# Kernel tuning notes

Measured on AMD Instinct MI355X. Metric: run time of the kernel, lower is better.

## Reference

```python
import jax, jax.numpy as jnp
import numpy as np

B, N, K, C_IN, C_OUT = 4, 8192, 16, 128, 128


def setup_inputs() -> dict:
    key = jax.random.key(0)
    k1, k2, k3 = jax.random.split(key, 3)
    x = jax.random.normal(k1, (B, N, C_IN), dtype=jnp.float32)
    edge_index = jax.random.randint(k2, (2, B, N, K), 0, N, dtype=jnp.int64)
    W = jax.random.normal(k3, (C_OUT, C_IN), dtype=jnp.float32) * (1.0 / np.sqrt(C_IN))
    b = jnp.zeros((C_OUT,), dtype=jnp.float32)
    eps = jnp.zeros((1,), dtype=jnp.float32)  # eps_init = 0.0
    return {"x": x, "edge_index": edge_index, "W": W, "b": b, "eps": eps}


def reference(x, edge_index, W, b, eps):
    # x: [B, N, C], edge_index: [2, B, N, K] -- use source index edge_index[0]
    idx = edge_index[0]                                   # [B, N, K]
    # gather neighbor features per batch: x_j[b,n,k,:] = x[b, idx[b,n,k], :]
    x_j = jax.vmap(lambda xb, ib: xb[ib])(x, idx)         # [B, N, K, C]
    agg = jnp.sum(x_j, axis=2)                            # sum over neighbors -> [B, N, C]
    h = (1.0 + eps) * x + agg                             # eps-scaled residual
    # MLP([in, out], act='relu'): single linear + relu on channel dim
    out = jax.nn.relu(jnp.einsum("bnc,oc->bno", h, W) + b)
    return out
```

## Files before the change

kernel.cpp:

```cpp
#include <hip/hip_runtime.h>
#include <stdint.h>

#define BATCH   4
#define NNODE   8192
#define KNBR    16
#define CIN     128
#define COUT    128
#define MB      32
#define THREADS 256
#define HS_STRIDE 136

typedef __attribute__((ext_vector_type(8))) short short8;
typedef __attribute__((ext_vector_type(4))) float f32x4;

__device__ __forceinline__ short bf16_rne(float f) {
    union { float f; uint32_t u; } v; v.f = f;
    return (short)((v.u + 0x7FFFu + ((v.u >> 16) & 1u)) >> 16);
}
__device__ __forceinline__ float bf16_f32(short s) {
    union { uint32_t u; float f; } v; v.u = ((uint32_t)(uint16_t)s) << 16;
    return v.f;
}

__global__ __launch_bounds__(256)
void cvt_bf16(const float* __restrict__ x, ushort* __restrict__ xb) {
    const int gid = blockIdx.x * 256 + threadIdx.x;
    const f32x4* xp = (const f32x4*)x + (size_t)gid * 2;
    f32x4 a = xp[0], c = xp[1];
    short8 s;
    s[0]=bf16_rne(a[0]); s[1]=bf16_rne(a[1]); s[2]=bf16_rne(a[2]); s[3]=bf16_rne(a[3]);
    s[4]=bf16_rne(c[0]); s[5]=bf16_rne(c[1]); s[6]=bf16_rne(c[2]); s[7]=bf16_rne(c[3]);
    ((short8*)xb)[gid] = s;
}

template<bool USEBF>
__global__ __launch_bounds__(THREADS, 2)
void gin_fused(const float*  __restrict__ x,
               const ushort* __restrict__ xb,
               const int*    __restrict__ eidx,
               const float*  __restrict__ W,
               const float*  __restrict__ bias,
               const float*  __restrict__ epsp,
               float*        __restrict__ out)
{
    __shared__ __align__(16) short h_s[MB * HS_STRIDE];

    const int tid = threadIdx.x;
    const int i   = blockIdx.x;
    const int xcd = i & 7;
    const int sub = i >> 3;
    const int b   = xcd >> 1;
    const int wbi = ((xcd & 1) << 7) | sub;
    const int n0  = wbi * MB;
    const int row0 = b * NNODE + n0;

    const float eps1 = 1.0f + epsp[0];

    {
        const int r  = tid >> 3;
        const int q  = tid & 7;
        const int n  = n0 + r;
        const int c0 = q * 16;
        const int* ip = eidx + ((size_t)b * NNODE + n) * KNBR;

        int js[KNBR];
        #pragma unroll
        for (int p = 0; p < 4; ++p) {
            int4 jv = *(const int4*)(ip + p * 4);
            js[p*4+0]=jv.x; js[p*4+1]=jv.y; js[p*4+2]=jv.z; js[p*4+3]=jv.w;
        }

        float acc[16];

        if constexpr (USEBF) {
            const ushort* xbb = xb + (size_t)b * NNODE * CIN;
            const ushort* xs  = xbb + (size_t)n * CIN + c0;
            short8 s0 = *(const short8*)xs, s1 = *(const short8*)(xs + 8);

            short8 t0[KNBR], t1[KNBR];
            #pragma unroll
            for (int k = 0; k < KNBR; ++k) {
                const ushort* xn = xbb + (size_t)js[k] * CIN + c0;
                t0[k] = *(const short8*)xn;
                t1[k] = *(const short8*)(xn + 8);
            }

            #pragma unroll
            for (int e = 0; e < 8; ++e) {
                acc[e]     = eps1 * bf16_f32(s0[e]);
                acc[8 + e] = eps1 * bf16_f32(s1[e]);
            }
            #pragma unroll
            for (int k = 0; k < KNBR; ++k) {
                #pragma unroll
                for (int e = 0; e < 8; ++e) {
                    acc[e]     += bf16_f32(t0[k][e]);
                    acc[8 + e] += bf16_f32(t1[k][e]);
                }
            }
        } else {
            const float* xbb = x + (size_t)b * NNODE * CIN;
            const float* xs  = xbb + (size_t)n * CIN + c0;
            #pragma unroll
            for (int p = 0; p < 4; ++p) {
                f32x4 v = *(const f32x4*)(xs + p * 4);
                acc[p*4+0]=eps1*v[0]; acc[p*4+1]=eps1*v[1]; acc[p*4+2]=eps1*v[2]; acc[p*4+3]=eps1*v[3];
            }
            #pragma unroll
            for (int k = 0; k < KNBR; ++k) {
                const float* xn = xbb + (size_t)js[k] * CIN + c0;
                #pragma unroll
                for (int p = 0; p < 4; ++p) {
                    f32x4 v = *(const f32x4*)(xn + p * 4);
                    acc[p*4+0]+=v[0]; acc[p*4+1]+=v[1]; acc[p*4+2]+=v[2]; acc[p*4+3]+=v[3];
                }
            }
        }

        short* hp = h_s + r * HS_STRIDE + c0;
        #pragma unroll
        for (int p = 0; p < 2; ++p) {
            short8 s;
            #pragma unroll
            for (int e = 0; e < 8; ++e) s[e] = bf16_rne(acc[p*8+e]);
            *(short8*)(hp + p * 8) = s;
        }
    }

    const int wave = tid >> 6;
    const int lane = tid & 63;
    const int l16  = lane & 15;
    const int lq   = lane >> 4;

    short8 bfrag[2][4];
    #pragma unroll
    for (int t = 0; t < 2; ++t) {
        const float* wp = W + (size_t)(wave * 32 + t * 16 + l16) * CIN;
        #pragma unroll
        for (int kb = 0; kb < 4; ++kb) {
            const float* wq = wp + kb * 32 + lq * 8;
            f32x4 f0 = *(const f32x4*)(wq);
            f32x4 f1 = *(const f32x4*)(wq + 4);
            short8 s;
            s[0]=bf16_rne(f0[0]); s[1]=bf16_rne(f0[1]); s[2]=bf16_rne(f0[2]); s[3]=bf16_rne(f0[3]);
            s[4]=bf16_rne(f1[0]); s[5]=bf16_rne(f1[1]); s[6]=bf16_rne(f1[2]); s[7]=bf16_rne(f1[3]);
            bfrag[t][kb] = s;
        }
    }
    const float bias0 = bias[wave * 32 + l16];
    const float bias1 = bias[wave * 32 + 16 + l16];

    __syncthreads();

    float* outb = out + (size_t)row0 * COUT;
    #pragma unroll
    for (int rt = 0; rt < MB / 16; ++rt) {
        const short* ap = h_s + (rt * 16 + l16) * HS_STRIDE + lq * 8;
        short8 afrag[4];
        #pragma unroll
        for (int kb = 0; kb < 4; ++kb)
            afrag[kb] = *(const short8*)(ap + kb * 32);

        #pragma unroll
        for (int t = 0; t < 2; ++t) {
            f32x4 acc = { 0.f, 0.f, 0.f, 0.f };
            #pragma unroll
            for (int kb = 0; kb < 4; ++kb)
                acc = __builtin_amdgcn_mfma_f32_16x16x32_bf16(afrag[kb], bfrag[t][kb], acc, 0, 0, 0);

            const float bv  = t ? bias1 : bias0;
            const int   col = wave * 32 + t * 16 + l16;
            #pragma unroll
            for (int ii = 0; ii < 4; ++ii) {
                const int row = rt * 16 + lq * 4 + ii;
                float v = acc[ii] + bv;
                outb[(size_t)row * COUT + col] = v > 0.f ? v : 0.f;
            }
        }
    }
}

extern "C" void kernel_launch(void* const* d_in, const int* in_sizes, int n_in,
                              void* d_out, int out_size, void* d_ws, size_t ws_size,
                              hipStream_t stream) {
    const float* x    = (const float*)d_in[0];
    const int*   eidx = (const int*)d_in[1];
    const float* W    = (const float*)d_in[2];
    const float* bias = (const float*)d_in[3];
    const float* eps  = (const float*)d_in[4];
    float*       out  = (float*)d_out;

    const size_t need = (size_t)BATCH * NNODE * CIN * sizeof(ushort);
    dim3 grid((BATCH * NNODE) / MB);

    if (ws_size >= need) {
        ushort* xb = (ushort*)d_ws;
        const int nelem = BATCH * NNODE * CIN;
        cvt_bf16<<<dim3(nelem / (256 * 8)), dim3(256), 0, stream>>>(x, xb);
        gin_fused<true><<<grid, dim3(THREADS), 0, stream>>>(x, xb, eidx, W, bias, eps, out);
    } else {
        gin_fused<false><<<grid, dim3(THREADS), 0, stream>>>(x, nullptr, eidx, W, bias, eps, out);
    }
}
```

Measured before the change: 95.73 us.

## Drop bf16 pre-conversion pass and gather fp32 neighbors in two batched halves

Removes the separate kernel that converted x to bf16 in workspace and always gathers neighbor rows directly in fp32. Neighbor loads are issued in two batches of eight rows, holding 32 vector registers of loads in flight before accumulating. This saves a full read and write pass over x and one kernel launch, but doubles the bytes fetched per gathered neighbor and raises register pressure.

```diff
diff --git a/kernel.cpp b/kernel.cpp
--- a/kernel.cpp
+++ b/kernel.cpp
@@ -17,31 +17,14 @@
     union { float f; uint32_t u; } v; v.f = f;
     return (short)((v.u + 0x7FFFu + ((v.u >> 16) & 1u)) >> 16);
 }
-__device__ __forceinline__ float bf16_f32(short s) {
-    union { uint32_t u; float f; } v; v.u = ((uint32_t)(uint16_t)s) << 16;
-    return v.f;
-}
 
-__global__ __launch_bounds__(256)
-void cvt_bf16(const float* __restrict__ x, ushort* __restrict__ xb) {
-    const int gid = blockIdx.x * 256 + threadIdx.x;
-    const f32x4* xp = (const f32x4*)x + (size_t)gid * 2;
-    f32x4 a = xp[0], c = xp[1];
-    short8 s;
-    s[0]=bf16_rne(a[0]); s[1]=bf16_rne(a[1]); s[2]=bf16_rne(a[2]); s[3]=bf16_rne(a[3]);
-    s[4]=bf16_rne(c[0]); s[5]=bf16_rne(c[1]); s[6]=bf16_rne(c[2]); s[7]=bf16_rne(c[3]);
-    ((short8*)xb)[gid] = s;
-}
-
-template<bool USEBF>
 __global__ __launch_bounds__(THREADS, 2)
-void gin_fused(const float*  __restrict__ x,
-               const ushort* __restrict__ xb,
-               const int*    __restrict__ eidx,
-               const float*  __restrict__ W,
-               const float*  __restrict__ bias,
-               const float*  __restrict__ epsp,
-               float*        __restrict__ out)
+void gin_fused_f32(const float*  __restrict__ x,
+                   const int*    __restrict__ eidx,
+                   const float*  __restrict__ W,
+                   const float*  __restrict__ bias,
+                   const float*  __restrict__ epsp,
+                   float*        __restrict__ out)
 {
     __shared__ __align__(16) short h_s[MB * HS_STRIDE];
 
@@ -70,49 +53,32 @@
             js[p*4+0]=jv.x; js[p*4+1]=jv.y; js[p*4+2]=jv.z; js[p*4+3]=jv.w;
         }
 
+        const float* xbb = x + (size_t)b * NNODE * CIN;
+        const float* xs  = xbb + (size_t)n * CIN + c0;
+
         float acc[16];
+        #pragma unroll
+        for (int p = 0; p < 4; ++p) {
+            f32x4 v = *(const f32x4*)(xs + p * 4);
+            acc[p*4+0]=eps1*v[0]; acc[p*4+1]=eps1*v[1];
+            acc[p*4+2]=eps1*v[2]; acc[p*4+3]=eps1*v[3];
+        }
 
-        if constexpr (USEBF) {
-            const ushort* xbb = xb + (size_t)b * NNODE * CIN;
-            const ushort* xs  = xbb + (size_t)n * CIN + c0;
-            short8 s0 = *(const short8*)xs, s1 = *(const short8*)(xs + 8);
-
-            short8 t0[KNBR], t1[KNBR];
+        #pragma unroll
+        for (int h = 0; h < 2; ++h) {
+            f32x4 t[8][4];
             #pragma unroll
-            for (int k = 0; k < KNBR; ++k) {
-                const ushort* xn = xbb + (size_t)js[k] * CIN + c0;
-                t0[k] = *(const short8*)xn;
-                t1[k] = *(const short8*)(xn + 8);
-            }
-
-            #pragma unroll
-            for (int e = 0; e < 8; ++e) {
-                acc[e]     = eps1 * bf16_f32(s0[e]);
-                acc[8 + e] = eps1 * bf16_f32(s1[e]);
+            for (int k = 0; k < 8; ++k) {
+                const float* xn = xbb + (size_t)js[h*8+k] * CIN + c0;
+                #pragma unroll
+                for (int p = 0; p < 4; ++p) t[k][p] = *(const f32x4*)(xn + p * 4);
             }
             #pragma unroll
-            for (int k = 0; k < KNBR; ++k) {
-                #pragma unroll
-                for (int e = 0; e < 8; ++e) {
-                    acc[e]     += bf16_f32(t0[k][e]);
-                    acc[8 + e] += bf16_f32(t1[k][e]);
-                }
-            }
-        } else {
-            const float* xbb = x + (size_t)b * NNODE * CIN;
-            const float* xs  = xbb + (size_t)n * CIN + c0;
-            #pragma unroll
-            for (int p = 0; p < 4; ++p) {
-                f32x4 v = *(const f32x4*)(xs + p * 4);
-                acc[p*4+0]=eps1*v[0]; acc[p*4+1]=eps1*v[1]; acc[p*4+2]=eps1*v[2]; acc[p*4+3]=eps1*v[3];
-            }
-            #pragma unroll
-            for (int k = 0; k < KNBR; ++k) {
-                const float* xn = xbb + (size_t)js[k] * CIN + c0;
+            for (int k = 0; k < 8; ++k) {
                 #pragma unroll
                 for (int p = 0; p < 4; ++p) {
-                    f32x4 v = *(const f32x4*)(xn + p * 4);
-                    acc[p*4+0]+=v[0]; acc[p*4+1]+=v[1]; acc[p*4+2]+=v[2]; acc[p*4+3]+=v[3];
+                    acc[p*4+0] += t[k][p][0]; acc[p*4+1] += t[k][p][1];
+                    acc[p*4+2] += t[k][p][2]; acc[p*4+3] += t[k][p][3];
                 }
             }
         }
@@ -190,15 +156,8 @@
     const float* eps  = (const float*)d_in[4];
     float*       out  = (float*)d_out;
 
-    const size_t need = (size_t)BATCH * NNODE * CIN * sizeof(ushort);
+    (void)d_ws; (void)ws_size;
+
     dim3 grid((BATCH * NNODE) / MB);
-
-    if (ws_size >= need) {
-        ushort* xb = (ushort*)d_ws;
-        const int nelem = BATCH * NNODE * CIN;
-        cvt_bf16<<<dim3(nelem / (256 * 8)), dim3(256), 0, stream>>>(x, xb);
-        gin_fused<true><<<grid, dim3(THREADS), 0, stream>>>(x, xb, eidx, W, bias, eps, out);
-    } else {
-        gin_fused<false><<<grid, dim3(THREADS), 0, stream>>>(x, nullptr, eidx, W, bias, eps, out);
-    }
+    gin_fused_f32<<<grid, dim3(THREADS), 0, stream>>>(x, eidx, W, bias, eps, out);
 }
```

New measurement: 113.6 us. 1.19x slower.

## Halve node tile to 16 rows, raise occupancy, add nontemporal loads/stores

Applied to the files above, without the earlier changes.

Shrinks the per-block node tile from 32 to 16 rows, so each thread gathers 8 channels instead of 16 and holds half as many neighbor vectors in registers. Launch bounds rise from 2 to 4 blocks per CU to allow more waves in flight to hide gather latency, and the XCD-aware block mapping is widened to match the doubled grid. The conversion kernel's input loads and the output stores are made nontemporal, and a sched_barrier keeps all gather loads issued before the accumulation. The trade-off is that every block now reloads and converts the full weight matrix for half as many rows, and there are more, smaller blocks.

```diff
diff --git a/kernel.cpp b/kernel.cpp
--- a/kernel.cpp
+++ b/kernel.cpp
@@ -6,7 +6,7 @@
 #define KNBR    16
 #define CIN     128
 #define COUT    128
-#define MB      32
+#define MB      16
 #define THREADS 256
 #define HS_STRIDE 136
 
@@ -26,7 +26,8 @@
 void cvt_bf16(const float* __restrict__ x, ushort* __restrict__ xb) {
     const int gid = blockIdx.x * 256 + threadIdx.x;
     const f32x4* xp = (const f32x4*)x + (size_t)gid * 2;
-    f32x4 a = xp[0], c = xp[1];
+    f32x4 a = __builtin_nontemporal_load(xp);
+    f32x4 c = __builtin_nontemporal_load(xp + 1);
     short8 s;
     s[0]=bf16_rne(a[0]); s[1]=bf16_rne(a[1]); s[2]=bf16_rne(a[2]); s[3]=bf16_rne(a[3]);
     s[4]=bf16_rne(c[0]); s[5]=bf16_rne(c[1]); s[6]=bf16_rne(c[2]); s[7]=bf16_rne(c[3]);
@@ -34,7 +35,7 @@
 }
 
 template<bool USEBF>
-__global__ __launch_bounds__(THREADS, 2)
+__global__ __launch_bounds__(THREADS, 4)
 void gin_fused(const float*  __restrict__ x,
                const ushort* __restrict__ xb,
                const int*    __restrict__ eidx,
@@ -50,17 +51,17 @@
     const int xcd = i & 7;
     const int sub = i >> 3;
     const int b   = xcd >> 1;
-    const int wbi = ((xcd & 1) << 7) | sub;
+    const int wbi = ((xcd & 1) << 8) | sub;
     const int n0  = wbi * MB;
     const int row0 = b * NNODE + n0;
 
     const float eps1 = 1.0f + epsp[0];
 
     {
-        const int r  = tid >> 3;
-        const int q  = tid & 7;
+        const int r  = tid >> 4;
+        const int q  = tid & 15;
         const int n  = n0 + r;
-        const int c0 = q * 16;
+        const int c0 = q * 8;
         const int* ip = eidx + ((size_t)b * NNODE + n) * KNBR;
 
         int js[KNBR];
@@ -70,61 +71,47 @@
             js[p*4+0]=jv.x; js[p*4+1]=jv.y; js[p*4+2]=jv.z; js[p*4+3]=jv.w;
         }
 
-        float acc[16];
+        float acc[8];
 
         if constexpr (USEBF) {
             const ushort* xbb = xb + (size_t)b * NNODE * CIN;
-            const ushort* xs  = xbb + (size_t)n * CIN + c0;
-            short8 s0 = *(const short8*)xs, s1 = *(const short8*)(xs + 8);
+            short8 s0 = *(const short8*)(xbb + (size_t)n * CIN + c0);
 
-            short8 t0[KNBR], t1[KNBR];
+            short8 t[KNBR];
             #pragma unroll
-            for (int k = 0; k < KNBR; ++k) {
-                const ushort* xn = xbb + (size_t)js[k] * CIN + c0;
-                t0[k] = *(const short8*)xn;
-                t1[k] = *(const short8*)(xn + 8);
-            }
+            for (int k = 0; k < KNBR; ++k)
+                t[k] = *(const short8*)(xbb + (size_t)js[k] * CIN + c0);
+            __builtin_amdgcn_sched_barrier(0);
 
             #pragma unroll
-            for (int e = 0; e < 8; ++e) {
-                acc[e]     = eps1 * bf16_f32(s0[e]);
-                acc[8 + e] = eps1 * bf16_f32(s1[e]);
-            }
+            for (int e = 0; e < 8; ++e) acc[e] = eps1 * bf16_f32(s0[e]);
             #pragma unroll
             for (int k = 0; k < KNBR; ++k) {
                 #pragma unroll
-                for (int e = 0; e < 8; ++e) {
-                    acc[e]     += bf16_f32(t0[k][e]);
-                    acc[8 + e] += bf16_f32(t1[k][e]);
-                }
+                for (int e = 0; e < 8; ++e) acc[e] += bf16_f32(t[k][e]);
             }
         } else {
             const float* xbb = x + (size_t)b * NNODE * CIN;
             const float* xs  = xbb + (size_t)n * CIN + c0;
+            f32x4 v0 = *(const f32x4*)(xs);
+            f32x4 v1 = *(const f32x4*)(xs + 4);
             #pragma unroll
-            for (int p = 0; p < 4; ++p) {
-                f32x4 v = *(const f32x4*)(xs + p * 4);
-                acc[p*4+0]=eps1*v[0]; acc[p*4+1]=eps1*v[1]; acc[p*4+2]=eps1*v[2]; acc[p*4+3]=eps1*v[3];
-            }
+            for (int e = 0; e < 4; ++e) { acc[e] = eps1*v0[e]; acc[4+e] = eps1*v1[e]; }
             #pragma unroll
             for (int k = 0; k < KNBR; ++k) {
                 const float* xn = xbb + (size_t)js[k] * CIN + c0;
+                f32x4 w0 = *(const f32x4*)(xn);
+                f32x4 w1 = *(const f32x4*)(xn + 4);
                 #pragma unroll
-                for (int p = 0; p < 4; ++p) {
-                    f32x4 v = *(const f32x4*)(xn + p * 4);
-                    acc[p*4+0]+=v[0]; acc[p*4+1]+=v[1]; acc[p*4+2]+=v[2]; acc[p*4+3]+=v[3];
-                }
+                for (int e = 0; e < 4; ++e) { acc[e] += w0[e]; acc[4+e] += w1[e]; }
             }
         }
 
         short* hp = h_s + r * HS_STRIDE + c0;
+        short8 s;
         #pragma unroll
-        for (int p = 0; p < 2; ++p) {
-            short8 s;
-            #pragma unroll
-            for (int e = 0; e < 8; ++e) s[e] = bf16_rne(acc[p*8+e]);
-            *(short8*)(hp + p * 8) = s;
-        }
+        for (int e = 0; e < 8; ++e) s[e] = bf16_rne(acc[e]);
+        *(short8*)hp = s;
     }
 
     const int wave = tid >> 6;
@@ -153,9 +140,8 @@
     __syncthreads();
 
     float* outb = out + (size_t)row0 * COUT;
-    #pragma unroll
-    for (int rt = 0; rt < MB / 16; ++rt) {
-        const short* ap = h_s + (rt * 16 + l16) * HS_STRIDE + lq * 8;
+    {
+        const short* ap = h_s + l16 * HS_STRIDE + lq * 8;
         short8 afrag[4];
         #pragma unroll
         for (int kb = 0; kb < 4; ++kb)
@@ -172,9 +158,10 @@
             const int   col = wave * 32 + t * 16 + l16;
             #pragma unroll
             for (int ii = 0; ii < 4; ++ii) {
-                const int row = rt * 16 + lq * 4 + ii;
+                const int row = lq * 4 + ii;
                 float v = acc[ii] + bv;
-                outb[(size_t)row * COUT + col] = v > 0.f ? v : 0.f;
+                v = v > 0.f ? v : 0.f;
+                __builtin_nontemporal_store(v, &outb[(size_t)row * COUT + col]);
             }
         }
     }
```

Result: slower. 101.7 us (+6.3%).

## Merge bf16 conversion and gather-GEMM into one persistent kernel with grid barrier

Applied to the files above, without the earlier changes.

Replaces the separate bf16 conversion kernel and the fused gather/MLP kernel with a single 512-block kernel. Each block converts its slice of x to bf16, waits on a global atomic barrier, then processes two 32-node tiles using the existing gather plus MFMA path. Nontemporal loads and stores are added for x, indices and output. The change removes one kernel launch and its inter-kernel gap. In exchange it relies on all 512 blocks being co-resident, since the software grid barrier deadlocks otherwise, and it halves the number of blocks that can hide gather latency.

```diff
diff --git a/kernel.cpp b/kernel.cpp
--- a/kernel.cpp
+++ b/kernel.cpp
@@ -6,12 +6,15 @@
 #define KNBR    16
 #define CIN     128
 #define COUT    128
-#define MB      32
 #define THREADS 256
+#define GRID    512
 #define HS_STRIDE 136
+
+#define XELEM   (BATCH * NNODE * CIN)
 
 typedef __attribute__((ext_vector_type(8))) short short8;
 typedef __attribute__((ext_vector_type(4))) float f32x4;
+typedef __attribute__((ext_vector_type(4))) int   i32x4;
 
 __device__ __forceinline__ short bf16_rne(float f) {
     union { float f; uint32_t u; } v; v.f = f;
@@ -22,108 +25,39 @@
     return v.f;
 }
 
-__global__ __launch_bounds__(256)
-void cvt_bf16(const float* __restrict__ x, ushort* __restrict__ xb) {
-    const int gid = blockIdx.x * 256 + threadIdx.x;
-    const f32x4* xp = (const f32x4*)x + (size_t)gid * 2;
-    f32x4 a = xp[0], c = xp[1];
-    short8 s;
-    s[0]=bf16_rne(a[0]); s[1]=bf16_rne(a[1]); s[2]=bf16_rne(a[2]); s[3]=bf16_rne(a[3]);
-    s[4]=bf16_rne(c[0]); s[5]=bf16_rne(c[1]); s[6]=bf16_rne(c[2]); s[7]=bf16_rne(c[3]);
-    ((short8*)xb)[gid] = s;
-}
-
-template<bool USEBF>
+__device__ unsigned long long g_bar;
+
 __global__ __launch_bounds__(THREADS, 2)
-void gin_fused(const float*  __restrict__ x,
-               const ushort* __restrict__ xb,
-               const int*    __restrict__ eidx,
-               const float*  __restrict__ W,
-               const float*  __restrict__ bias,
-               const float*  __restrict__ epsp,
-               float*        __restrict__ out)
+void gin_mono(const float* __restrict__ x,
+              const int*   __restrict__ eidx,
+              const float* __restrict__ W,
+              const float* __restrict__ bias,
+              const float* __restrict__ epsp,
+              ushort*      __restrict__ xb,
+              float*       __restrict__ out)
 {
-    __shared__ __align__(16) short h_s[MB * HS_STRIDE];
-
-    const int tid = threadIdx.x;
-    const int i   = blockIdx.x;
-    const int xcd = i & 7;
-    const int sub = i >> 3;
-    const int b   = xcd >> 1;
-    const int wbi = ((xcd & 1) << 7) | sub;
-    const int n0  = wbi * MB;
-    const int row0 = b * NNODE + n0;
-
-    const float eps1 = 1.0f + epsp[0];
+    __shared__ __align__(16) short h_s[32 * HS_STRIDE];
+
+    const int tid  = threadIdx.x;
+    const int i    = blockIdx.x;
+    const int xcd  = i & 7;
+    const int sub  = i >> 3;
+    const int b    = xcd >> 1;
+    const int half = xcd & 1;
+    const int chunk = half * 64 + sub;
 
     {
-        const int r  = tid >> 3;
-        const int q  = tid & 7;
-        const int n  = n0 + r;
-        const int c0 = q * 16;
-        const int* ip = eidx + ((size_t)b * NNODE + n) * KNBR;
-
-        int js[KNBR];
-        #pragma unroll
-        for (int p = 0; p < 4; ++p) {
-            int4 jv = *(const int4*)(ip + p * 4);
-            js[p*4+0]=jv.x; js[p*4+1]=jv.y; js[p*4+2]=jv.z; js[p*4+3]=jv.w;
-        }
-
-        float acc[16];
-
-        if constexpr (USEBF) {
-            const ushort* xbb = xb + (size_t)b * NNODE * CIN;
-            const ushort* xs  = xbb + (size_t)n * CIN + c0;
-            short8 s0 = *(const short8*)xs, s1 = *(const short8*)(xs + 8);
-
-            short8 t0[KNBR], t1[KNBR];
-            #pragma unroll
-            for (int k = 0; k < KNBR; ++k) {
-                const ushort* xn = xbb + (size_t)js[k] * CIN + c0;
-                t0[k] = *(const short8*)xn;
-                t1[k] = *(const short8*)(xn + 8);
-            }
-
-            #pragma unroll
-            for (int e = 0; e < 8; ++e) {
-                acc[e]     = eps1 * bf16_f32(s0[e]);
-                acc[8 + e] = eps1 * bf16_f32(s1[e]);
-            }
-            #pragma unroll
-            for (int k = 0; k < KNBR; ++k) {
-                #pragma unroll
-                for (int e = 0; e < 8; ++e) {
-                    acc[e]     += bf16_f32(t0[k][e]);
-                    acc[8 + e] += bf16_f32(t1[k][e]);
-                }
-            }
-        } else {
-            const float* xbb = x + (size_t)b * NNODE * CIN;
-            const float* xs  = xbb + (size_t)n * CIN + c0;
-            #pragma unroll
-            for (int p = 0; p < 4; ++p) {
-                f32x4 v = *(const f32x4*)(xs + p * 4);
-                acc[p*4+0]=eps1*v[0]; acc[p*4+1]=eps1*v[1]; acc[p*4+2]=eps1*v[2]; acc[p*4+3]=eps1*v[3];
-            }
-            #pragma unroll
-            for (int k = 0; k < KNBR; ++k) {
-                const float* xn = xbb + (size_t)js[k] * CIN + c0;
-                #pragma unroll
-                for (int p = 0; p < 4; ++p) {
-                    f32x4 v = *(const f32x4*)(xn + p * 4);
-                    acc[p*4+0]+=v[0]; acc[p*4+1]+=v[1]; acc[p*4+2]+=v[2]; acc[p*4+3]+=v[3];
-                }
-            }
-        }
-
-        short* hp = h_s + r * HS_STRIDE + c0;
-        #pragma unroll
-        for (int p = 0; p < 2; ++p) {
+        const size_t base = ((size_t)b * NNODE + (size_t)chunk * 64) * CIN;
+        const float*  xs = x  + base + tid * 32;
+        ushort*       xd = xb + base + tid * 32;
+        #pragma unroll
+        for (int g = 0; g < 4; ++g) {
+            f32x4 a = __builtin_nontemporal_load((const f32x4*)(xs + g * 8));
+            f32x4 c = __builtin_nontemporal_load((const f32x4*)(xs + g * 8 + 4));
             short8 s;
-            #pragma unroll
-            for (int e = 0; e < 8; ++e) s[e] = bf16_rne(acc[p*8+e]);
-            *(short8*)(hp + p * 8) = s;
+            s[0]=bf16_rne(a[0]); s[1]=bf16_rne(a[1]); s[2]=bf16_rne(a[2]); s[3]=bf16_rne(a[3]);
+            s[4]=bf16_rne(c[0]); s[5]=bf16_rne(c[1]); s[6]=bf16_rne(c[2]); s[7]=bf16_rne(c[3]);
+            *(short8*)(xd + g * 8) = s;
         }
     }
 
@@ -149,27 +83,192 @@
     }
     const float bias0 = bias[wave * 32 + l16];
     const float bias1 = bias[wave * 32 + 16 + l16];
-
+    const float eps1  = 1.0f + epsp[0];
+
+    __threadfence();
     __syncthreads();
-
+    if (tid == 0) {
+        unsigned long long t = atomicAdd(&g_bar, 1ULL);
+        unsigned long long target = (t / GRID + 1ULL) * GRID;
+        while (__hip_atomic_load(&g_bar, __ATOMIC_RELAXED, __HIP_MEMORY_SCOPE_AGENT) < target)
+            __builtin_amdgcn_s_sleep(8);
+    }
+    __syncthreads();
+    __threadfence();
+
+    #pragma unroll 1
+    for (int tt = 0; tt < 2; ++tt) {
+        const int n0   = chunk * 64 + tt * 32;
+        const int row0 = b * NNODE + n0;
+
+        {
+            const int r  = tid >> 3;
+            const int q  = tid & 7;
+            const int n  = n0 + r;
+            const int c0 = q * 16;
+            const int* ip = eidx + ((size_t)b * NNODE + n) * KNBR;
+
+            int js[KNBR];
+            #pragma unroll
+            for (int p = 0; p < 4; ++p) {
+                i32x4 jv = __builtin_nontemporal_load((const i32x4*)(ip + p * 4));
+                js[p*4+0]=jv.x; js[p*4+1]=jv.y; js[p*4+2]=jv.z; js[p*4+3]=jv.w;
+            }
+
+            const ushort* xbb = xb + (size_t)b * NNODE * CIN;
+            const ushort* xs  = xbb + (size_t)n * CIN + c0;
+            short8 s0 = *(const short8*)xs, s1 = *(const short8*)(xs + 8);
+
+            short8 t0[KNBR], t1[KNBR];
+            #pragma unroll
+            for (int k = 0; k < KNBR; ++k) {
+                const ushort* xn = xbb + (size_t)js[k] * CIN + c0;
+                t0[k] = *(const short8*)xn;
+                t1[k] = *(const short8*)(xn + 8);
+            }
+
+            float acc[16];
+            #pragma unroll
+            for (int e = 0; e < 8; ++e) {
+                acc[e]     = eps1 * bf16_f32(s0[e]);
+                acc[8 + e] = eps1 * bf16_f32(s1[e]);
+            }
+            #pragma unroll
+            for (int k = 0; k < KNBR; ++k) {
+                #pragma unroll
+                for (int e = 0; e < 8; ++e) {
+                    acc[e]     += bf16_f32(t0[k][e]);
+                    acc[8 + e] += bf16_f32(t1[k][e]);
+                }
+            }
+
+            short* hp = h_s + r * HS_STRIDE + c0;
+            #pragma unroll
+            for (int p = 0; p < 2; ++p) {
+                short8 s;
+                #pragma unroll
+                for (int e = 0; e < 8; ++e) s[e] = bf16_rne(acc[p*8+e]);
+                *(short8*)(hp + p * 8) = s;
+            }
+        }
+
+        __syncthreads();
+
+        float* outb = out + (size_t)row0 * COUT;
+        #pragma unroll
+        for (int rt = 0; rt < 2; ++rt) {
+            const short* ap = h_s + (rt * 16 + l16) * HS_STRIDE + lq * 8;
+            short8 afrag[4];
+            #pragma unroll
+            for (int kb = 0; kb < 4; ++kb)
+                afrag[kb] = *(const short8*)(ap + kb * 32);
+
+            #pragma unroll
+            for (int t = 0; t < 2; ++t) {
+                f32x4 acc = { 0.f, 0.f, 0.f, 0.f };
+                #pragma unroll
+                for (int kb = 0; kb < 4; ++kb)
+                    acc = __builtin_amdgcn_mfma_f32_16x16x32_bf16(afrag[kb], bfrag[t][kb], acc, 0, 0, 0);
+
+                const float bv  = t ? bias1 : bias0;
+                const int   col = wave * 32 + t * 16 + l16;
+                #pragma unroll
+                for (int ii = 0; ii < 4; ++ii) {
+                    const int row = rt * 16 + lq * 4 + ii;
+                    float v = acc[ii] + bv;
+                    v = v > 0.f ? v : 0.f;
+                    __builtin_nontemporal_store(v, &outb[(size_t)row * COUT + col]);
+                }
+            }
+        }
+
+        __syncthreads();
+    }
+}
+
+__global__ __launch_bounds__(THREADS, 2)
+void gin_fallback(const float* __restrict__ x, const int* __restrict__ eidx,
+                  const float* __restrict__ W, const float* __restrict__ bias,
+                  const float* __restrict__ epsp, float* __restrict__ out)
+{
+    __shared__ __align__(16) short h_s[32 * HS_STRIDE];
+    const int tid = threadIdx.x;
+    const int i   = blockIdx.x;
+    const int xcd = i & 7, sub = i >> 3;
+    const int b   = xcd >> 1;
+    const int wbi = ((xcd & 1) << 7) | sub;
+    const int n0  = wbi * 32;
+    const int row0 = b * NNODE + n0;
+    const float eps1 = 1.0f + epsp[0];
+    {
+        const int r = tid >> 3, q = tid & 7, n = n0 + r, c0 = q * 16;
+        const int* ip = eidx + ((size_t)b * NNODE + n) * KNBR;
+        int js[KNBR];
+        #pragma unroll
+        for (int p = 0; p < 4; ++p) {
+            i32x4 jv = *(const i32x4*)(ip + p * 4);
+            js[p*4+0]=jv.x; js[p*4+1]=jv.y; js[p*4+2]=jv.z; js[p*4+3]=jv.w;
+        }
+        float acc[16];
+        const float* xbb = x + (size_t)b * NNODE * CIN;
+        const float* xs  = xbb + (size_t)n * CIN + c0;
+        #pragma unroll
+        for (int p = 0; p < 4; ++p) {
+            f32x4 v = *(const f32x4*)(xs + p * 4);
+            acc[p*4+0]=eps1*v[0]; acc[p*4+1]=eps1*v[1]; acc[p*4+2]=eps1*v[2]; acc[p*4+3]=eps1*v[3];
+        }
+        #pragma unroll
+        for (int k = 0; k < KNBR; ++k) {
+            const float* xn = xbb + (size_t)js[k] * CIN + c0;
+            #pragma unroll
+            for (int p = 0; p < 4; ++p) {
+                f32x4 v = *(const f32x4*)(xn + p * 4);
+                acc[p*4+0]+=v[0]; acc[p*4+1]+=v[1]; acc[p*4+2]+=v[2]; acc[p*4+3]+=v[3];
+            }
+        }
+        short* hp = h_s + r * HS_STRIDE + c0;
+        #pragma unroll
+        for (int p = 0; p < 2; ++p) {
+            short8 s;
+            #pragma unroll
+            for (int e = 0; e < 8; ++e) s[e] = bf16_rne(acc[p*8+e]);
+            *(short8*)(hp + p * 8) = s;
+        }
+    }
+    const int wave = tid >> 6, lane = tid & 63, l16 = lane & 15, lq = lane >> 4;
+    short8 bfrag[2][4];
+    #pragma unroll
+    for (int t = 0; t < 2; ++t) {
+        const float* wp = W + (size_t)(wave * 32 + t * 16 + l16) * CIN;
+        #pragma unroll
+        for (int kb = 0; kb < 4; ++kb) {
+            const float* wq = wp + kb * 32 + lq * 8;
+            f32x4 f0 = *(const f32x4*)(wq);
+            f32x4 f1 = *(const f32x4*)(wq + 4);
+            short8 s;
+            s[0]=bf16_rne(f0[0]); s[1]=bf16_rne(f0[1]); s[2]=bf16_rne(f0[2]); s[3]=bf16_rne(f0[3]);
+            s[4]=bf16_rne(f1[0]); s[5]=bf16_rne(f1[1]); s[6]=bf16_rne(f1[2]); s[7]=bf16_rne(f1[3]);
+            bfrag[t][kb] = s;
+        }
+    }
+    const float bias0 = bias[wave * 32 + l16];
+    const float bias1 = bias[wave * 32 + 16 + l16];
+    __syncthreads();
     float* outb = out + (size_t)row0 * COUT;
     #pragma unroll
-    for (int rt = 0; rt < MB / 16; ++rt) {
+    for (int rt = 0; rt < 2; ++rt) {
         const short* ap = h_s + (rt * 16 + l16) * HS_STRIDE + lq * 8;
         short8 afrag[4];
         #pragma unroll
-        for (int kb = 0; kb < 4; ++kb)
-            afrag[kb] = *(const short8*)(ap + kb * 32);
-
+        for (int kb = 0; kb < 4; ++kb) afrag[kb] = *(const short8*)(ap + kb * 32);
         #pragma unroll
         for (int t = 0; t < 2; ++t) {
             f32x4 acc = { 0.f, 0.f, 0.f, 0.f };
             #pragma unroll
             for (int kb = 0; kb < 4; ++kb)
                 acc = __builtin_amdgcn_mfma_f32_16x16x32_bf16(afrag[kb], bfrag[t][kb], acc, 0, 0, 0);
-
-            const float bv  = t ? bias1 : bias0;
-            const int   col = wave * 32 + t * 16 + l16;
+            const float bv = t ? bias1 : bias0;
+            const int col = wave * 32 + t * 16 + l16;
             #pragma unroll
             for (int ii = 0; ii < 4; ++ii) {
                 const int row = rt * 16 + lq * 4 + ii;
@@ -190,15 +289,12 @@
     const float* eps  = (const float*)d_in[4];
     float*       out  = (float*)d_out;
 
-    const size_t need = (size_t)BATCH * NNODE * CIN * sizeof(ushort);
-    dim3 grid((BATCH * NNODE) / MB);
+    const size_t need = (size_t)XELEM * sizeof(ushort);
 
     if (ws_size >= need) {
         ushort* xb = (ushort*)d_ws;
-        const int nelem = BATCH * NNODE * CIN;
-        cvt_bf16<<<dim3(nelem / (256 * 8)), dim3(256), 0, stream>>>(x, xb);
-        gin_fused<true><<<grid, dim3(THREADS), 0, stream>>>(x, xb, eidx, W, bias, eps, out);
+        gin_mono<<<dim3(GRID), dim3(THREADS), 0, stream>>>(x, eidx, W, bias, eps, xb, out);
     } else {
-        gin_fused<false><<<grid, dim3(THREADS), 0, stream>>>(x, nullptr, eidx, W, bias, eps, out);
-    }
-}
+        gin_fallback<<<dim3((BATCH * NNODE) / 32), dim3(THREADS), 0, stream>>>(x, eidx, W, bias, eps, out);
+    }
+}
```

Result: slower. 226.2 us (+136.3%).
